# Optimization experiments

Measured on AMD Instinct MI355X. Metric: run time of the kernel, lower is better.

The kernel has to match this reference:

```python
import jax, jax.numpy as jnp
import numpy as np
from jax import lax

EPS = 1e-5
BETA = 0.2  # commitment loss weight


def _conv(x, w, b, stride=2, pad=1):
    # torch Conv2d(k=4, s=2, p=1), NCHW / OIHW
    y = lax.conv_general_dilated(x, w, (stride, stride), [(pad, pad), (pad, pad)],
                                 dimension_numbers=('NCHW', 'OIHW', 'NCHW'))
    return y + b[None, :, None, None]


def _convT(x, w, b):
    # torch ConvTranspose2d(k=4, s=2, p=1): dilated conv with flipped kernel,
    # effective pad = k - 1 - p = 2. w is torch layout [in, out, kH, kW].
    wt = jnp.flip(w, (2, 3)).transpose(1, 0, 2, 3)  # -> [out, in, kH, kW]
    y = lax.conv_general_dilated(x, wt, (1, 1), [(2, 2), (2, 2)], lhs_dilation=(2, 2),
                                 dimension_numbers=('NCHW', 'OIHW', 'NCHW'))
    return y + b[None, :, None, None]


def _bn(x, g, b):
    # BatchNorm2d in training mode: per-channel batch statistics (biased var)
    m = x.mean((0, 2, 3), keepdims=True)
    v = x.var((0, 2, 3), keepdims=True)
    xn = (x - m) * lax.rsqrt(v + EPS)
    return g[None, :, None, None] * xn + b[None, :, None, None]


def _forward(x, enc_w1, enc_b1, enc_w2, enc_b2, enc_w3, enc_b3,
             enc_g1, enc_be1, enc_g2, enc_be2, enc_g3, enc_be3,
             codebook,
             dec_w1, dec_b1, dec_w2, dec_b2, dec_w3, dec_b3,
             dec_g1, dec_be1, dec_g2, dec_be2, dec_g3, dec_be3):
    # ---- Encoder: [B,1,256,256] -> [B,32,32,32] ----
    h = jax.nn.relu(_bn(_conv(x, enc_w1, enc_b1), enc_g1, enc_be1))
    h = jax.nn.relu(_bn(_conv(h, enc_w2, enc_b2), enc_g2, enc_be2))
    q_in = jax.nn.relu(_bn(_conv(h, enc_w3, enc_b3), enc_g3, enc_be3))

    B, C, H, W = q_in.shape
    # ---- Quantiser: cdist + argmin + codebook gather ----
    z = q_in.transpose(0, 2, 3, 1).reshape(B, H * W, C)  # [B, HW, C]
    # squared euclidean distance (same argmin as torch.cdist)
    d2 = (jnp.sum(z * z, -1, keepdims=True)
          - 2.0 * jnp.einsum('bnc,kc->bnk', z, codebook)
          + jnp.sum(codebook * codebook, -1))  # [B, HW, K]
    idx = jnp.argmin(d2, axis=-1)  # [B, HW] int
    q_out = codebook[idx].reshape(B, H, W, C).transpose(0, 3, 1, 2)  # [B,C,H,W]

    commitment = jnp.mean((lax.stop_gradient(q_out) - q_in) ** 2)
    codebook_l = jnp.mean((q_out - lax.stop_gradient(q_in)) ** 2)
    quant_loss = codebook_l + BETA * commitment
    # straight-through estimator
    q_st = q_in + lax.stop_gradient(q_out - q_in)
    encoding_indices = idx.reshape(-1, H, W)

    # ---- Decoder: [B,32,32,32] -> [B,1,256,256] ----
    d = jax.nn.relu(_bn(_convT(q_st, dec_w1, dec_b1), dec_g1, dec_be1))
    d = jax.nn.relu(_bn(_convT(d, dec_w2, dec_b2), dec_g2, dec_be2))
    out = _bn(_convT(d, dec_w3, dec_b3), dec_g3, dec_be3)

    recon = jnp.mean((x - out) ** 2)
    total_loss = quant_loss + recon
    return out, total_loss, encoding_indices


def setup_inputs() -> dict:
    key = jax.random.key(0)
    ks = jax.random.split(key, 12)
    rn = lambda k, s, sc=0.05: jax.random.normal(k, s, jnp.float32) * sc
    inp = {
        'x': jax.random.normal(ks[0], (64, 1, 256, 256), jnp.float32),
        'enc_w1': rn(ks[1], (16, 1, 4, 4)),  'enc_b1': jnp.zeros((16,), jnp.float32),
        'enc_w2': rn(ks[2], (16, 16, 4, 4)), 'enc_b2': jnp.zeros((16,), jnp.float32),
        'enc_w3': rn(ks[3], (32, 16, 4, 4)), 'enc_b3': jnp.zeros((32,), jnp.float32),
        'enc_g1': jnp.ones((16,), jnp.float32), 'enc_be1': jnp.zeros((16,), jnp.float32),
        'enc_g2': jnp.ones((16,), jnp.float32), 'enc_be2': jnp.zeros((16,), jnp.float32),
        'enc_g3': jnp.ones((32,), jnp.float32), 'enc_be3': jnp.zeros((32,), jnp.float32),
        'codebook': jax.random.normal(ks[4], (512, 32), jnp.float32),  # nn.Embedding ~ N(0,1)
        'dec_w1': rn(ks[5], (32, 16, 4, 4)), 'dec_b1': jnp.zeros((16,), jnp.float32),  # [in,out,kH,kW]
        'dec_w2': rn(ks[6], (16, 16, 4, 4)), 'dec_b2': jnp.zeros((16,), jnp.float32),
        'dec_w3': rn(ks[7], (16, 1, 4, 4)),  'dec_b3': jnp.zeros((1,), jnp.float32),
        'dec_g1': jnp.ones((16,), jnp.float32), 'dec_be1': jnp.zeros((16,), jnp.float32),
        'dec_g2': jnp.ones((16,), jnp.float32), 'dec_be2': jnp.zeros((16,), jnp.float32),
        'dec_g3': jnp.ones((1,), jnp.float32),  'dec_be3': jnp.zeros((1,), jnp.float32),
    }
    return inp


def reference(x, enc_w1, enc_b1, enc_w2, enc_b2, enc_w3, enc_b3,
              enc_g1, enc_be1, enc_g2, enc_be2, enc_g3, enc_be3,
              codebook,
              dec_w1, dec_b1, dec_w2, dec_b2, dec_w3, dec_b3,
              dec_g1, dec_be1, dec_g2, dec_be2, dec_g3, dec_be3):
    return _forward(x, enc_w1, enc_b1, enc_w2, enc_b2, enc_w3, enc_b3,
                    enc_g1, enc_be1, enc_g2, enc_be2, enc_g3, enc_be3,
                    codebook,
                    dec_w1, dec_b1, dec_w2, dec_b2, dec_w3, dec_b3,
                    dec_g1, dec_be1, dec_g2, dec_be2, dec_g3, dec_be3)
```

## Files before the change

kernel.cpp:

```cpp
#include <hip/hip_runtime.h>

#define BLK 256


__device__ __forceinline__ void block_stats2(float s, float q, float* partOut) {
  __shared__ float red2[2][4];
  const int lane = threadIdx.x & 63;
  const int wv   = threadIdx.x >> 6;
#pragma unroll
  for (int off = 32; off > 0; off >>= 1) {
    s += __shfl_down(s, off, 64);
    q += __shfl_down(q, off, 64);
  }
  if (lane == 0) { red2[0][wv] = s; red2[1][wv] = q; }
  __syncthreads();
  if (threadIdx.x == 0) {
    partOut[0] = red2[0][0] + red2[0][1] + red2[0][2] + red2[0][3];
    partOut[1] = red2[1][0] + red2[1][1] + red2[1][2] + red2[1][3];
  }
}


__global__ __launch_bounds__(BLK) void twc_k(const float* __restrict__ w,
                                             float* __restrict__ wt,
                                             int CI, int CO) {
  const int total = CI * CO * 16;
  for (int i = threadIdx.x; i < total; i += BLK) {
    const int co = i % CO;
    const int rest = i / CO;
    const int kw = rest & 3, kh = (rest >> 2) & 3, ci = rest >> 4;
    wt[i] = w[(co * CI + ci) * 16 + kh * 4 + kw];
  }
}

__global__ __launch_bounds__(BLK) void twt_k(const float* __restrict__ w,
                                             float* __restrict__ wt,
                                             int CI, int CO) {
  const int total = CI * CO * 16;
  for (int i = threadIdx.x; i < total; i += BLK) {
    const int co = i % CO;
    const int rest = i / CO;
    const int kw = rest & 3, kh = (rest >> 2) & 3, ci = rest >> 4;
    wt[i] = w[(ci * CO + co) * 16 + kh * 4 + kw];
  }
}


template<int CI, int CO, int CGN, int PW, int HIN, int WIN, bool BN_IN>
__global__ __launch_bounds__(64 * PW * CGN) void conv_cg(
    const float* __restrict__ in, const float* __restrict__ wt,
    const float* __restrict__ bias,
    const float* __restrict__ scIn, const float* __restrict__ shIn,
    float* __restrict__ out, float* __restrict__ part)
{
  constexpr int HOUT = HIN / 2, WOUT = WIN / 2;
  constexpr int COG = CO / CGN;
  const int lane = threadIdx.x & 63;
  const int w    = threadIdx.x >> 6;
  const int pw   = w & (PW - 1);
  const int cg   = w / PW;
  const int co0  = __builtin_amdgcn_readfirstlane(cg * COG);

  float sc[CI], sh[CI];
  if constexpr (BN_IN) {
#pragma unroll
    for (int ci = 0; ci < CI; ++ci) { sc[ci] = scIn[ci]; sh[ci] = shIn[ci]; }
  }

  const int pos = blockIdx.x * (64 * PW) + pw * 64 + lane;
  const int ow  = pos % WOUT;
  const int oh  = (pos / WOUT) % HOUT;
  const int b   = pos / (WOUT * HOUT);

  float acc[COG];
#pragma unroll
  for (int j = 0; j < COG; ++j) acc[j] = bias[co0 + j];

  const float* inb = in + (size_t)b * CI * HIN * WIN;

#pragma unroll
  for (int kh = 0; kh < 4; ++kh) {
    const int ih = oh * 2 - 1 + kh;
    if ((unsigned)ih < (unsigned)HIN) {
#pragma unroll
      for (int kw = 0; kw < 4; ++kw) {
        const int iw = ow * 2 - 1 + kw;
        if ((unsigned)iw < (unsigned)WIN) {
#pragma unroll 2
          for (int ci = 0; ci < CI; ++ci) {
            float v = inb[(ci * HIN + ih) * WIN + iw];
            if constexpr (BN_IN) v = fmaxf(fmaf(sc[ci], v, sh[ci]), 0.f);
            const float* wrow = wt + ((ci * 4 + kh) * 4 + kw) * CO + co0;
#pragma unroll
            for (int j = 0; j < COG; ++j)
              acc[j] = fmaf(v, wrow[j], acc[j]);
          }
        }
      }
    }
  }

#pragma unroll
  for (int j = 0; j < COG; ++j)
    out[((size_t)(b * CO + co0 + j) * HOUT + oh) * WOUT + ow] = acc[j];

  float s[COG], q[COG];
#pragma unroll
  for (int j = 0; j < COG; ++j) { s[j] = acc[j]; q[j] = acc[j] * acc[j]; }
#pragma unroll
  for (int off = 32; off > 0; off >>= 1)
#pragma unroll
    for (int j = 0; j < COG; ++j) {
      s[j] += __shfl_down(s[j], off, 64);
      q[j] += __shfl_down(q[j], off, 64);
    }
  __shared__ float red[CGN * PW][COG][2];
  if (lane == 0) {
#pragma unroll
    for (int j = 0; j < COG; ++j) { red[w][j][0] = s[j]; red[w][j][1] = q[j]; }
  }
  __syncthreads();
  if (threadIdx.x < CO) {
    const int co = threadIdx.x;
    const int cg2 = co / COG, j = co % COG;
    float ss = 0.f, qq = 0.f;
#pragma unroll
    for (int p2 = 0; p2 < PW; ++p2) {
      ss += red[cg2 * PW + p2][j][0];
      qq += red[cg2 * PW + p2][j][1];
    }
    part[(size_t)blockIdx.x * CO * 2 + co * 2]     = ss;
    part[(size_t)blockIdx.x * CO * 2 + co * 2 + 1] = qq;
  }
}


template<int CI, int CGN, int PW, int HIN, bool BN_IN>
__global__ __launch_bounds__(64 * PW * CGN) void convTq_cg(
    const float* __restrict__ in, const float* __restrict__ wt,
    const float* __restrict__ bias,
    const float* __restrict__ scIn, const float* __restrict__ shIn,
    float* __restrict__ out, float* __restrict__ part)
{
  constexpr int WIN = HIN, HOUT = 2 * HIN, WOUT = 2 * WIN;
  constexpr int COG = 16 / CGN;
  const int lane = threadIdx.x & 63;
  const int w    = threadIdx.x >> 6;
  const int pw   = w & (PW - 1);
  const int cg   = w / PW;
  const int co0  = __builtin_amdgcn_readfirstlane(cg * COG);

  const int q_  = blockIdx.x * (64 * PW) + pw * 64 + lane;
  const int qw  = q_ % WIN;
  const int qh  = (q_ / WIN) % HIN;
  const int b   = q_ / (WIN * HIN);

  constexpr int KH[2][2] = {{1, 3}, {0, 2}};
  constexpr int PR[2][2] = {{1, 0}, {2, 1}};

  float acc[2][2][COG];
#pragma unroll
  for (int j = 0; j < COG; ++j) {
    const float bv = bias[co0 + j];
    acc[0][0][j] = bv; acc[0][1][j] = bv;
    acc[1][0][j] = bv; acc[1][1][j] = bv;
  }

  const float* inb = in + (size_t)b * CI * HIN * WIN;

#pragma unroll 2
  for (int ci = 0; ci < CI; ++ci) {
    float sci, shi;
    if constexpr (BN_IN) { sci = scIn[ci]; shi = shIn[ci]; }
    const float* base = inb + ci * HIN * WIN;
    float v[3][3];
#pragma unroll
    for (int pr = 0; pr < 3; ++pr) {
      const int ih = qh - 1 + pr;
      const bool okr = (unsigned)ih < (unsigned)HIN;
#pragma unroll
      for (int pc = 0; pc < 3; ++pc) {
        const int iw = qw - 1 + pc;
        float val = 0.f;
        if (okr && (unsigned)iw < (unsigned)WIN) {
          val = base[ih * WIN + iw];
          if constexpr (BN_IN) val = fmaxf(fmaf(sci, val, shi), 0.f);
        }
        v[pr][pc] = val;
      }
    }
#pragma unroll
    for (int py = 0; py < 2; ++py)
#pragma unroll
      for (int tr = 0; tr < 2; ++tr) {
        const int kh = KH[py][tr], pr_ = PR[py][tr];
#pragma unroll
        for (int px = 0; px < 2; ++px)
#pragma unroll
          for (int tc = 0; tc < 2; ++tc) {
            const int kw = KH[px][tc], pc_ = PR[px][tc];
            const float* wrow = wt + ((ci * 4 + kh) * 4 + kw) * 16 + co0;
            const float pv = v[pr_][pc_];
#pragma unroll
            for (int j = 0; j < COG; ++j)
              acc[py][px][j] = fmaf(pv, wrow[j], acc[py][px][j]);
          }
      }
  }

  float* ob = out + (size_t)b * 16 * HOUT * WOUT;
#pragma unroll
  for (int j = 0; j < COG; ++j)
#pragma unroll
    for (int py = 0; py < 2; ++py) {
      float2 o; o.x = acc[py][0][j]; o.y = acc[py][1][j];
      *(float2*)&ob[((size_t)(co0 + j) * HOUT + 2 * qh + py) * WOUT + 2 * qw] = o;
    }

  float s[COG], q[COG];
#pragma unroll
  for (int j = 0; j < COG; ++j) {
    float a = acc[0][0][j] + acc[0][1][j] + acc[1][0][j] + acc[1][1][j];
    float qq = acc[0][0][j] * acc[0][0][j];
    qq = fmaf(acc[0][1][j], acc[0][1][j], qq);
    qq = fmaf(acc[1][0][j], acc[1][0][j], qq);
    qq = fmaf(acc[1][1][j], acc[1][1][j], qq);
    s[j] = a; q[j] = qq;
  }
#pragma unroll
  for (int off = 32; off > 0; off >>= 1)
#pragma unroll
    for (int j = 0; j < COG; ++j) {
      s[j] += __shfl_down(s[j], off, 64);
      q[j] += __shfl_down(q[j], off, 64);
    }
  __shared__ float red[CGN * PW][COG][2];
  if (lane == 0) {
#pragma unroll
    for (int j = 0; j < COG; ++j) { red[w][j][0] = s[j]; red[w][j][1] = q[j]; }
  }
  __syncthreads();
  if (threadIdx.x < 16) {
    const int co = threadIdx.x;
    const int cg2 = co / COG, j = co % COG;
    float ss = 0.f, qq = 0.f;
#pragma unroll
    for (int p2 = 0; p2 < PW; ++p2) {
      ss += red[cg2 * PW + p2][j][0];
      qq += red[cg2 * PW + p2][j][1];
    }
    part[(size_t)blockIdx.x * 32 + co * 2]     = ss;
    part[(size_t)blockIdx.x * 32 + co * 2 + 1] = qq;
  }
}


__global__ __launch_bounds__(BLK) void convT3q_k(
    const float* __restrict__ in, const float* __restrict__ w,
    const float* __restrict__ bias,
    const float* __restrict__ scIn, const float* __restrict__ shIn,
    float* __restrict__ out, float* __restrict__ part)
{
  __shared__ float wl[256];
  wl[threadIdx.x] = w[threadIdx.x];
  float sc[16], sh[16];
#pragma unroll
  for (int ci = 0; ci < 16; ++ci) { sc[ci] = scIn[ci]; sh[ci] = shIn[ci]; }
  const float b0 = bias[0];
  __syncthreads();

  const int idx = blockIdx.x * BLK + threadIdx.x;
  const int tx = idx & 63;
  const int ty = (idx >> 6) & 63;
  const int b  = idx >> 12;
  const int i0 = ty * 2, j0 = tx * 2;

  constexpr int TAP[4][4] = {{1,1,3,0},{0,2,2,1},{1,2,3,1},{0,3,2,2}};

  float acc[4][4];
#pragma unroll
  for (int r = 0; r < 4; ++r)
#pragma unroll
    for (int c = 0; c < 4; ++c) acc[r][c] = b0;

  const float* inb = in + (size_t)b * 16 * 16384;

#pragma unroll 4
  for (int ci = 0; ci < 16; ++ci) {
    const float sci = sc[ci], shi = sh[ci];
    const float* base = inb + ci * 16384;
    float v[4][4];
#pragma unroll
    for (int pr = 0; pr < 4; ++pr) {
      const int ih = i0 - 1 + pr;
      const bool okr = (unsigned)ih < 128u;
#pragma unroll
      for (int pc = 0; pc < 4; ++pc) {
        const int iw = j0 - 1 + pc;
        float val = 0.f;
        if (okr && (unsigned)iw < 128u)
          val = fmaxf(fmaf(sci, base[ih * 128 + iw], shi), 0.f);
        v[pr][pc] = val;
      }
    }
    const float4 w0 = *(const float4*)&wl[ci * 16 + 0];
    const float4 w1 = *(const float4*)&wl[ci * 16 + 4];
    const float4 w2 = *(const float4*)&wl[ci * 16 + 8];
    const float4 w3 = *(const float4*)&wl[ci * 16 + 12];
    const float wg[16] = {w0.x,w0.y,w0.z,w0.w, w1.x,w1.y,w1.z,w1.w,
                          w2.x,w2.y,w2.z,w2.w, w3.x,w3.y,w3.z,w3.w};
#pragma unroll
    for (int r = 0; r < 4; ++r) {
      const int k1r = TAP[r][0], p1r = TAP[r][1], k2r = TAP[r][2], p2r = TAP[r][3];
#pragma unroll
      for (int c = 0; c < 4; ++c) {
        const int k1c = TAP[c][0], p1c = TAP[c][1], k2c = TAP[c][2], p2c = TAP[c][3];
        float a = acc[r][c];
        a = fmaf(v[p1r][p1c], wg[k1r * 4 + k1c], a);
        a = fmaf(v[p1r][p2c], wg[k1r * 4 + k2c], a);
        a = fmaf(v[p2r][p1c], wg[k2r * 4 + k1c], a);
        a = fmaf(v[p2r][p2c], wg[k2r * 4 + k2c], a);
        acc[r][c] = a;
      }
    }
  }

  float* ob = out + (size_t)b * 65536;
#pragma unroll
  for (int r = 0; r < 4; ++r) {
    float4 o;
    o.x = acc[r][0]; o.y = acc[r][1]; o.z = acc[r][2]; o.w = acc[r][3];
    *(float4*)&ob[(ty * 4 + r) * 256 + tx * 4] = o;
  }

  float s = 0.f, q = 0.f;
#pragma unroll
  for (int r = 0; r < 4; ++r)
#pragma unroll
    for (int c = 0; c < 4; ++c) { s += acc[r][c]; q = fmaf(acc[r][c], acc[r][c], q); }
  block_stats2(s, q, part + (size_t)blockIdx.x * 2);
}


template<int C>
__global__ __launch_bounds__(BLK) void stats_k(
    const float* __restrict__ part, int nB, double N,
    const float* __restrict__ g, const float* __restrict__ be,
    float* __restrict__ sc, float* __restrict__ sh)
{
  const int c = blockIdx.x;
  double s0 = 0.0, s1 = 0.0;
  for (int i = threadIdx.x; i < nB; i += BLK) {
    s0 += (double)part[(size_t)i * C * 2 + c * 2];
    s1 += (double)part[(size_t)i * C * 2 + c * 2 + 1];
  }
  __shared__ double lds[8];
  const int lane = threadIdx.x & 63, wv = threadIdx.x >> 6;
#pragma unroll
  for (int off = 32; off > 0; off >>= 1) {
    s0 += __shfl_down(s0, off, 64);
    s1 += __shfl_down(s1, off, 64);
  }
  if (lane == 0) { lds[wv * 2] = s0; lds[wv * 2 + 1] = s1; }
  __syncthreads();
  if (threadIdx.x == 0) {
    s0 = lds[0] + lds[2] + lds[4] + lds[6];
    s1 = lds[1] + lds[3] + lds[5] + lds[7];
    const double mean = s0 / N;
    const double var  = s1 / N - mean * mean;
    const double inv  = 1.0 / sqrt(var + 1e-5);
    sc[c] = (float)((double)g[c] * inv);
    sh[c] = (float)((double)be[c] - mean * (double)g[c] * inv);
  }
}


__global__ __launch_bounds__(BLK) void cbn_k(const float* __restrict__ cbg,
                                             float* __restrict__ cbn)
{
  const int k = blockIdx.x * BLK + threadIdx.x;
  float s = 0.f;
#pragma unroll
  for (int c = 0; c < 32; ++c) {
    const float x = cbg[k * 32 + c];
    s = fmaf(x, x, s);
  }
  cbn[k] = s;
}

__global__ __launch_bounds__(BLK) void quantp_k(
    const float* __restrict__ y3, const float* __restrict__ cbg,
    const float* __restrict__ cbnG,
    const float* __restrict__ sc, const float* __restrict__ sh,
    float* __restrict__ bd, int* __restrict__ bki)
{
  __shared__ float cb[64 * 32];
  __shared__ float cbnl[64];
  const int pblk  = blockIdx.x & 63;
  const int chunk = blockIdx.x >> 6;
  for (int i = threadIdx.x; i < 2048; i += BLK) cb[i] = cbg[chunk * 2048 + i];
  if (threadIdx.x < 64) cbnl[threadIdx.x] = cbnG[chunk * 64 + threadIdx.x];
  __syncthreads();

  const int pos0 = pblk * 1024 + threadIdx.x;

  float z[4][32];
#pragma unroll
  for (int c = 0; c < 32; ++c) {
    const float s_ = sc[c], h_ = sh[c];
#pragma unroll
    for (int j = 0; j < 4; ++j) {
      const int pos = pos0 + j * 256;
      const int bb = pos >> 10, pp = pos & 1023;
      z[j][c] = fmaxf(fmaf(s_, y3[((size_t)(bb * 32 + c)) * 1024 + pp], h_), 0.f);
    }
  }

  float best[4] = {3.402823466e38f, 3.402823466e38f, 3.402823466e38f, 3.402823466e38f};
  int   bk[4]   = {0, 0, 0, 0};

  for (int k = 0; k < 64; ++k) {
    const float4* row = (const float4*)&cb[k * 32];
    float d[4] = {0.f, 0.f, 0.f, 0.f};
#pragma unroll
    for (int c4 = 0; c4 < 8; ++c4) {
      const float4 cc = row[c4];
#pragma unroll
      for (int j = 0; j < 4; ++j) {
        d[j] = fmaf(z[j][c4 * 4 + 0], cc.x, d[j]);
        d[j] = fmaf(z[j][c4 * 4 + 1], cc.y, d[j]);
        d[j] = fmaf(z[j][c4 * 4 + 2], cc.z, d[j]);
        d[j] = fmaf(z[j][c4 * 4 + 3], cc.w, d[j]);
      }
    }
    const float cl = cbnl[k];
    const int kk = chunk * 64 + k;
#pragma unroll
    for (int j = 0; j < 4; ++j) {
      const float dd = cl - 2.f * d[j];
      if (dd < best[j]) { best[j] = dd; bk[j] = kk; }
    }
  }

#pragma unroll
  for (int j = 0; j < 4; ++j) {
    const int pos = pos0 + j * 256;
    bd[chunk * 65536 + pos]  = best[j];
    bki[chunk * 65536 + pos] = bk[j];
  }
}

__global__ __launch_bounds__(BLK) void quantm_k(
    const float* __restrict__ y3, const float* __restrict__ cbg,
    const float* __restrict__ sc, const float* __restrict__ sh,
    const float* __restrict__ bd, const int* __restrict__ bki,
    float* __restrict__ qout, float* __restrict__ idx_out,
    float* __restrict__ pq)
{
  const int pos = blockIdx.x * BLK + threadIdx.x;
  float best = 3.402823466e38f;
  int bk = 0;
#pragma unroll
  for (int s = 0; s < 8; ++s) {
    const float d = bd[s * 65536 + pos];
    const int   k = bki[s * 65536 + pos];
    if (d < best) { best = d; bk = k; }
  }

  const int b = pos >> 10, p = pos & 1023;
  const float4* qrow = (const float4*)(cbg + (size_t)bk * 32);
  float msd = 0.f;
#pragma unroll
  for (int c4 = 0; c4 < 8; ++c4) {
    const float4 q4 = qrow[c4];
    const float qv[4] = {q4.x, q4.y, q4.z, q4.w};
#pragma unroll
    for (int u = 0; u < 4; ++u) {
      const int c = c4 * 4 + u;
      const float v  = y3[((size_t)(b * 32 + c)) * 1024 + p];
      const float zz = fmaxf(fmaf(sc[c], v, sh[c]), 0.f);
      const float qq = qv[u];
      qout[((size_t)(b * 32 + c)) * 1024 + p] = zz + (qq - zz);
      const float df = qq - zz;
      msd = fmaf(df, df, msd);
    }
  }
  idx_out[pos] = (float)bk;
  block_stats2(msd, 0.f, pq + (size_t)blockIdx.x * 2);
}


__global__ __launch_bounds__(BLK) void final4_k(
    const float* __restrict__ y6, const float* __restrict__ x,
    const float* __restrict__ sc, const float* __restrict__ sh,
    float* __restrict__ out, float* __restrict__ pr)
{
  const size_t i = ((size_t)blockIdx.x * BLK + threadIdx.x) * 4;
  const float s0 = sc[0], h0 = sh[0];
  const float4 yv = *(const float4*)(y6 + i);
  const float4 xv = *(const float4*)(x + i);
  float4 ov;
  ov.x = fmaf(s0, yv.x, h0);
  ov.y = fmaf(s0, yv.y, h0);
  ov.z = fmaf(s0, yv.z, h0);
  ov.w = fmaf(s0, yv.w, h0);
  *(float4*)(out + i) = ov;
  const float d0 = xv.x - ov.x, d1 = xv.y - ov.y, d2 = xv.z - ov.z, d3 = xv.w - ov.w;
  float s = d0 * d0;
  s = fmaf(d1, d1, s);
  s = fmaf(d2, d2, s);
  s = fmaf(d3, d3, s);
  block_stats2(s, 0.f, pr + (size_t)blockIdx.x * 2);
}


__global__ __launch_bounds__(BLK) void loss_k(
    const float* __restrict__ pq, const float* __restrict__ pr,
    float* __restrict__ lossOut)
{
  double s = 0.0, r = 0.0;
  for (int i = threadIdx.x; i < 256; i += BLK)  s += (double)pq[i * 2];
  for (int i = threadIdx.x; i < 4096; i += BLK) r += (double)pr[i * 2];
  __shared__ double lds[8];
  const int lane = threadIdx.x & 63, wv = threadIdx.x >> 6;
#pragma unroll
  for (int off = 32; off > 0; off >>= 1) {
    s += __shfl_down(s, off, 64);
    r += __shfl_down(r, off, 64);
  }
  if (lane == 0) { lds[wv * 2] = s; lds[wv * 2 + 1] = r; }
  __syncthreads();
  if (threadIdx.x == 0) {
    s = lds[0] + lds[2] + lds[4] + lds[6];
    r = lds[1] + lds[3] + lds[5] + lds[7];
    lossOut[0] = (float)(1.2 * (s / 2097152.0) + r / 4194304.0);
  }
}


extern "C" void kernel_launch(void* const* d_in, const int* in_sizes, int n_in,
                              void* d_out, int out_size, void* d_ws, size_t ws_size,
                              hipStream_t stream) {
  const float* x    = (const float*)d_in[0];
  const float* ew1  = (const float*)d_in[1];
  const float* eb1  = (const float*)d_in[2];
  const float* ew2  = (const float*)d_in[3];
  const float* eb2  = (const float*)d_in[4];
  const float* ew3  = (const float*)d_in[5];
  const float* eb3  = (const float*)d_in[6];
  const float* eg1  = (const float*)d_in[7];
  const float* ebe1 = (const float*)d_in[8];
  const float* eg2  = (const float*)d_in[9];
  const float* ebe2 = (const float*)d_in[10];
  const float* eg3  = (const float*)d_in[11];
  const float* ebe3 = (const float*)d_in[12];
  const float* cbk  = (const float*)d_in[13];
  const float* dw1  = (const float*)d_in[14];
  const float* db1  = (const float*)d_in[15];
  const float* dw2  = (const float*)d_in[16];
  const float* db2  = (const float*)d_in[17];
  const float* dw3  = (const float*)d_in[18];
  const float* db3  = (const float*)d_in[19];
  const float* dg1  = (const float*)d_in[20];
  const float* dbe1 = (const float*)d_in[21];
  const float* dg2  = (const float*)d_in[22];
  const float* dbe2 = (const float*)d_in[23];
  const float* dg3  = (const float*)d_in[24];
  const float* dbe3 = (const float*)d_in[25];

  float* ws = (float*)d_ws;
  float* outp = (float*)d_out;

  float* SC = ws;
  float* SH = ws + 192;
  float* P1 = ws + 1024;
  float* P2 = ws + 132096;
  float* P3 = ws + 164864;
  float* P4 = ws + 181248;
  float* P5 = ws + 214016;
  float* P6 = ws + 345088;
  float* Pq = ws + 377856;
  float* Pr = ws + 378368;
  float* CBN = ws + 411648;
  float* WT1  = ws + 412160;
  float* WT2  = WT1 + 256;
  float* WT3  = WT2 + 4096;
  float* WTD1 = WT3 + 8192;
  float* WTD2 = WTD1 + 8192;

  float* y1 = ws + 524288;
  float* y2 = y1 + 16777216;
  float* y3 = y2 + 4194304;
  float* qo = y3 + 2097152;
  float* y6 = qo + 2097152;
  float* y4 = y2;
  float* y5 = y1;
  float* bd  = y2;
  int*   bki = (int*)(y2 + 524288);

  float* sc1 = SC + 0,  *sh1 = SH + 0;
  float* sc2 = SC + 32, *sh2 = SH + 32;
  float* sc3 = SC + 64, *sh3 = SH + 64;
  float* sc4 = SC + 96, *sh4 = SH + 96;
  float* sc5 = SC + 128,*sh5 = SH + 128;
  float* sc6 = SC + 160,*sh6 = SH + 160;

  twc_k<<<1, BLK, 0, stream>>>(ew1, WT1, 1, 16);
  twc_k<<<1, BLK, 0, stream>>>(ew2, WT2, 16, 16);
  twc_k<<<1, BLK, 0, stream>>>(ew3, WT3, 16, 32);
  twt_k<<<1, BLK, 0, stream>>>(dw1, WTD1, 32, 16);
  twt_k<<<1, BLK, 0, stream>>>(dw2, WTD2, 16, 16);
  cbn_k<<<2, BLK, 0, stream>>>(cbk, CBN);

  conv_cg<1, 16, 2, 4, 256, 256, false><<<4096, 512, 0, stream>>>(x,  WT1, eb1, nullptr, nullptr, y1, P1);
  stats_k<16><<<16, BLK, 0, stream>>>(P1, 4096, 1048576.0, eg1, ebe1, sc1, sh1);
  conv_cg<16, 16, 2, 4, 128, 128, true><<<1024, 512, 0, stream>>>(y1, WT2, eb2, sc1, sh1, y2, P2);
  stats_k<16><<<16, BLK, 0, stream>>>(P2, 1024, 262144.0, eg2, ebe2, sc2, sh2);
  conv_cg<16, 32, 4, 4, 64, 64, true><<<256, 1024, 0, stream>>>(y2, WT3, eb3, sc2, sh2, y3, P3);
  stats_k<32><<<32, BLK, 0, stream>>>(P3, 256, 65536.0, eg3, ebe3, sc3, sh3);

  quantp_k<<<512, BLK, 0, stream>>>(y3, cbk, CBN, sc3, sh3, bd, bki);
  quantm_k<<<256, BLK, 0, stream>>>(y3, cbk, sc3, sh3, bd, bki, qo, outp + 4194305, Pq);

  convTq_cg<32, 4, 1, 32, false><<<1024, 256, 0, stream>>>(qo, WTD1, db1, nullptr, nullptr, y4, P4);
  stats_k<16><<<16, BLK, 0, stream>>>(P4, 1024, 262144.0, dg1, dbe1, sc4, sh4);
  convTq_cg<16, 2, 2, 64, true><<<2048, 256, 0, stream>>>(y4, WTD2, db2, sc4, sh4, y5, P5);
  stats_k<16><<<16, BLK, 0, stream>>>(P5, 2048, 1048576.0, dg2, dbe2, sc5, sh5);
  convT3q_k<<<1024, BLK, 0, stream>>>(y5, dw3, db3, sc5, sh5, y6, P6);
  stats_k<1><<<1, BLK, 0, stream>>>(P6, 1024, 4194304.0, dg3, dbe3, sc6, sh6);

  final4_k<<<4096, BLK, 0, stream>>>(y6, x, sc6, sh6, outp, Pr);
  loss_k<<<1, BLK, 0, stream>>>(Pq, Pr, outp + 4194304);
}
```

Measured before the change: 621.8 us.

## Compute two output rows per thread in encoder convs and decoder convT

Adds conv_cg2 and convTq2_cg variants where each thread computes two output rows (or a 2x2x2 output block for the transposed conv). Overlapping input rows are loaded once and reused across both, and grid sizes are halved to match. This cuts redundant global input loads and BN-apply work per output, at the cost of more accumulator registers and fewer blocks. convT3q_k also drops its LDS weight staging and the barrier, reading weights directly from global memory, which relies on uniform scalar or cached loads.

```diff
diff --git a/kernel.cpp b/kernel.cpp
--- a/kernel.cpp
+++ b/kernel.cpp
@@ -47,6 +47,119 @@
 
 
 template<int CI, int CO, int CGN, int PW, int HIN, int WIN, bool BN_IN>
+__global__ __launch_bounds__(64 * PW * CGN) void conv_cg2(
+    const float* __restrict__ in, const float* __restrict__ wt,
+    const float* __restrict__ bias,
+    const float* __restrict__ scIn, const float* __restrict__ shIn,
+    float* __restrict__ out, float* __restrict__ part)
+{
+  constexpr int HOUT = HIN / 2, WOUT = WIN / 2;
+  constexpr int COG = CO / CGN;
+  const int lane = threadIdx.x & 63;
+  const int w    = threadIdx.x >> 6;
+  const int pw   = w & (PW - 1);
+  const int cg   = w / PW;
+  const int co0  = __builtin_amdgcn_readfirstlane(cg * COG);
+
+  float sc[CI], sh[CI];
+  if constexpr (BN_IN) {
+#pragma unroll
+    for (int ci = 0; ci < CI; ++ci) { sc[ci] = scIn[ci]; sh[ci] = shIn[ci]; }
+  }
+
+  const int pp  = blockIdx.x * (64 * PW) + pw * 64 + lane;
+  const int ow  = pp % WOUT;
+  const int op  = (pp / WOUT) % (HOUT / 2);
+  const int b   = pp / (WOUT * (HOUT / 2));
+  const int ih0 = 4 * op - 1;
+  const int iw0 = 2 * ow - 1;
+
+  float acc[2][COG];
+#pragma unroll
+  for (int j = 0; j < COG; ++j) {
+    const float bv = bias[co0 + j];
+    acc[0][j] = bv; acc[1][j] = bv;
+  }
+
+  const float* inb = in + (size_t)b * CI * HIN * WIN;
+
+#pragma unroll 2
+  for (int ci = 0; ci < CI; ++ci) {
+    float sci, shi;
+    if constexpr (BN_IN) { sci = sc[ci]; shi = sh[ci]; }
+    const float* base = inb + ci * HIN * WIN;
+    float v[6][4];
+#pragma unroll
+    for (int pr = 0; pr < 6; ++pr) {
+      const int ih = ih0 + pr;
+      const bool okr = (unsigned)ih < (unsigned)HIN;
+#pragma unroll
+      for (int pc = 0; pc < 4; ++pc) {
+        const int iw = iw0 + pc;
+        float val = 0.f;
+        if (okr && (unsigned)iw < (unsigned)WIN) {
+          val = base[ih * WIN + iw];
+          if constexpr (BN_IN) val = fmaxf(fmaf(sci, val, shi), 0.f);
+        }
+        v[pr][pc] = val;
+      }
+    }
+#pragma unroll
+    for (int r2 = 0; r2 < 2; ++r2)
+#pragma unroll
+      for (int kh = 0; kh < 4; ++kh)
+#pragma unroll
+        for (int kw = 0; kw < 4; ++kw) {
+          const float pv = v[2 * r2 + kh][kw];
+          const float* wrow = wt + ((ci * 4 + kh) * 4 + kw) * CO + co0;
+#pragma unroll
+          for (int j = 0; j < COG; ++j)
+            acc[r2][j] = fmaf(pv, wrow[j], acc[r2][j]);
+        }
+  }
+
+#pragma unroll
+  for (int r2 = 0; r2 < 2; ++r2)
+#pragma unroll
+    for (int j = 0; j < COG; ++j)
+      out[((size_t)(b * CO + co0 + j) * HOUT + 2 * op + r2) * WOUT + ow] = acc[r2][j];
+
+  float s[COG], q[COG];
+#pragma unroll
+  for (int j = 0; j < COG; ++j) {
+    s[j] = acc[0][j] + acc[1][j];
+    float qq = acc[0][j] * acc[0][j];
+    q[j] = fmaf(acc[1][j], acc[1][j], qq);
+  }
+#pragma unroll
+  for (int off = 32; off > 0; off >>= 1)
+#pragma unroll
+    for (int j = 0; j < COG; ++j) {
+      s[j] += __shfl_down(s[j], off, 64);
+      q[j] += __shfl_down(q[j], off, 64);
+    }
+  __shared__ float red[CGN * PW][COG][2];
+  if (lane == 0) {
+#pragma unroll
+    for (int j = 0; j < COG; ++j) { red[w][j][0] = s[j]; red[w][j][1] = q[j]; }
+  }
+  __syncthreads();
+  if (threadIdx.x < CO) {
+    const int co = threadIdx.x;
+    const int cg2 = co / COG, j = co % COG;
+    float ss = 0.f, qq = 0.f;
+#pragma unroll
+    for (int p2 = 0; p2 < PW; ++p2) {
+      ss += red[cg2 * PW + p2][j][0];
+      qq += red[cg2 * PW + p2][j][1];
+    }
+    part[(size_t)blockIdx.x * CO * 2 + co * 2]     = ss;
+    part[(size_t)blockIdx.x * CO * 2 + co * 2 + 1] = qq;
+  }
+}
+
+
+template<int CI, int CO, int CGN, int PW, int HIN, int WIN, bool BN_IN>
 __global__ __launch_bounds__(64 * PW * CGN) void conv_cg(
     const float* __restrict__ in, const float* __restrict__ wt,
     const float* __restrict__ bias,
@@ -255,19 +368,150 @@
 }
 
 
+template<int CI, int CGN, int PW, int HIN, bool BN_IN>
+__global__ __launch_bounds__(64 * PW * CGN) void convTq2_cg(
+    const float* __restrict__ in, const float* __restrict__ wt,
+    const float* __restrict__ bias,
+    const float* __restrict__ scIn, const float* __restrict__ shIn,
+    float* __restrict__ out, float* __restrict__ part)
+{
+  constexpr int WIN = HIN, HOUT = 2 * HIN, WOUT = 2 * WIN;
+  constexpr int COG = 16 / CGN;
+  const int lane = threadIdx.x & 63;
+  const int w    = threadIdx.x >> 6;
+  const int pw   = w & (PW - 1);
+  const int cg   = w / PW;
+  const int co0  = __builtin_amdgcn_readfirstlane(cg * COG);
+
+  const int q_  = blockIdx.x * (64 * PW) + pw * 64 + lane;
+  const int qw  = q_ % WIN;
+  const int tq  = (q_ / WIN) % (HIN / 2);
+  const int b   = q_ / (WIN * (HIN / 2));
+  const int qh0 = 2 * tq;
+
+  constexpr int KH[2][2] = {{1, 3}, {0, 2}};
+  constexpr int PR[2][2] = {{1, 0}, {2, 1}};
+
+  float acc[2][2][2][COG];
+#pragma unroll
+  for (int j = 0; j < COG; ++j) {
+    const float bv = bias[co0 + j];
+#pragma unroll
+    for (int t2 = 0; t2 < 2; ++t2)
+#pragma unroll
+      for (int py = 0; py < 2; ++py)
+#pragma unroll
+        for (int px = 0; px < 2; ++px) acc[t2][py][px][j] = bv;
+  }
+
+  const float* inb = in + (size_t)b * CI * HIN * WIN;
+
+#pragma unroll 2
+  for (int ci = 0; ci < CI; ++ci) {
+    float sci, shi;
+    if constexpr (BN_IN) { sci = scIn[ci]; shi = shIn[ci]; }
+    const float* base = inb + ci * HIN * WIN;
+    float v[4][3];
+#pragma unroll
+    for (int pr = 0; pr < 4; ++pr) {
+      const int ih = qh0 - 1 + pr;
+      const bool okr = (unsigned)ih < (unsigned)HIN;
+#pragma unroll
+      for (int pc = 0; pc < 3; ++pc) {
+        const int iw = qw - 1 + pc;
+        float val = 0.f;
+        if (okr && (unsigned)iw < (unsigned)WIN) {
+          val = base[ih * WIN + iw];
+          if constexpr (BN_IN) val = fmaxf(fmaf(sci, val, shi), 0.f);
+        }
+        v[pr][pc] = val;
+      }
+    }
+#pragma unroll
+    for (int t2 = 0; t2 < 2; ++t2)
+#pragma unroll
+      for (int py = 0; py < 2; ++py)
+#pragma unroll
+        for (int tr = 0; tr < 2; ++tr) {
+          const int kh = KH[py][tr], pr_ = t2 + PR[py][tr];
+#pragma unroll
+          for (int px = 0; px < 2; ++px)
+#pragma unroll
+            for (int tc = 0; tc < 2; ++tc) {
+              const int kw = KH[px][tc], pc_ = PR[px][tc];
+              const float* wrow = wt + ((ci * 4 + kh) * 4 + kw) * 16 + co0;
+              const float pv = v[pr_][pc_];
+#pragma unroll
+              for (int j = 0; j < COG; ++j)
+                acc[t2][py][px][j] = fmaf(pv, wrow[j], acc[t2][py][px][j]);
+            }
+        }
+  }
+
+  float* ob = out + (size_t)b * 16 * HOUT * WOUT;
+#pragma unroll
+  for (int j = 0; j < COG; ++j)
+#pragma unroll
+    for (int t2 = 0; t2 < 2; ++t2)
+#pragma unroll
+      for (int py = 0; py < 2; ++py) {
+        float2 o; o.x = acc[t2][py][0][j]; o.y = acc[t2][py][1][j];
+        *(float2*)&ob[((size_t)(co0 + j) * HOUT + 2 * (qh0 + t2) + py) * WOUT + 2 * qw] = o;
+      }
+
+  float s[COG], q[COG];
+#pragma unroll
+  for (int j = 0; j < COG; ++j) {
+    float a = 0.f, qq = 0.f;
+#pragma unroll
+    for (int t2 = 0; t2 < 2; ++t2)
+#pragma unroll
+      for (int py = 0; py < 2; ++py)
+#pragma unroll
+        for (int px = 0; px < 2; ++px) {
+          a += acc[t2][py][px][j];
+          qq = fmaf(acc[t2][py][px][j], acc[t2][py][px][j], qq);
+        }
+    s[j] = a; q[j] = qq;
+  }
+#pragma unroll
+  for (int off = 32; off > 0; off >>= 1)
+#pragma unroll
+    for (int j = 0; j < COG; ++j) {
+      s[j] += __shfl_down(s[j], off, 64);
+      q[j] += __shfl_down(q[j], off, 64);
+    }
+  __shared__ float red[CGN * PW][COG][2];
+  if (lane == 0) {
+#pragma unroll
+    for (int j = 0; j < COG; ++j) { red[w][j][0] = s[j]; red[w][j][1] = q[j]; }
+  }
+  __syncthreads();
+  if (threadIdx.x < 16) {
+    const int co = threadIdx.x;
+    const int cg2 = co / COG, j = co % COG;
+    float ss = 0.f, qq = 0.f;
+#pragma unroll
+    for (int p2 = 0; p2 < PW; ++p2) {
+      ss += red[cg2 * PW + p2][j][0];
+      qq += red[cg2 * PW + p2][j][1];
+    }
+    part[(size_t)blockIdx.x * 32 + co * 2]     = ss;
+    part[(size_t)blockIdx.x * 32 + co * 2 + 1] = qq;
+  }
+}
+
+
 __global__ __launch_bounds__(BLK) void convT3q_k(
     const float* __restrict__ in, const float* __restrict__ w,
     const float* __restrict__ bias,
     const float* __restrict__ scIn, const float* __restrict__ shIn,
     float* __restrict__ out, float* __restrict__ part)
 {
-  __shared__ float wl[256];
-  wl[threadIdx.x] = w[threadIdx.x];
   float sc[16], sh[16];
 #pragma unroll
   for (int ci = 0; ci < 16; ++ci) { sc[ci] = scIn[ci]; sh[ci] = shIn[ci]; }
   const float b0 = bias[0];
-  __syncthreads();
 
   const int idx = blockIdx.x * BLK + threadIdx.x;
   const int tx = idx & 63;
@@ -303,12 +547,7 @@
         v[pr][pc] = val;
       }
     }
-    const float4 w0 = *(const float4*)&wl[ci * 16 + 0];
-    const float4 w1 = *(const float4*)&wl[ci * 16 + 4];
-    const float4 w2 = *(const float4*)&wl[ci * 16 + 8];
-    const float4 w3 = *(const float4*)&wl[ci * 16 + 12];
-    const float wg[16] = {w0.x,w0.y,w0.z,w0.w, w1.x,w1.y,w1.z,w1.w,
-                          w2.x,w2.y,w2.z,w2.w, w3.x,w3.y,w3.z,w3.w};
+    const float* wg = w + ci * 16;
 #pragma unroll
     for (int r = 0; r < 4; ++r) {
       const int k1r = TAP[r][0], p1r = TAP[r][1], k2r = TAP[r][2], p2r = TAP[r][3];
@@ -612,10 +851,10 @@
   twt_k<<<1, BLK, 0, stream>>>(dw2, WTD2, 16, 16);
   cbn_k<<<2, BLK, 0, stream>>>(cbk, CBN);
 
-  conv_cg<1, 16, 2, 4, 256, 256, false><<<4096, 512, 0, stream>>>(x,  WT1, eb1, nullptr, nullptr, y1, P1);
-  stats_k<16><<<16, BLK, 0, stream>>>(P1, 4096, 1048576.0, eg1, ebe1, sc1, sh1);
-  conv_cg<16, 16, 2, 4, 128, 128, true><<<1024, 512, 0, stream>>>(y1, WT2, eb2, sc1, sh1, y2, P2);
-  stats_k<16><<<16, BLK, 0, stream>>>(P2, 1024, 262144.0, eg2, ebe2, sc2, sh2);
+  conv_cg2<1, 16, 2, 4, 256, 256, false><<<2048, 512, 0, stream>>>(x,  WT1, eb1, nullptr, nullptr, y1, P1);
+  stats_k<16><<<16, BLK, 0, stream>>>(P1, 2048, 1048576.0, eg1, ebe1, sc1, sh1);
+  conv_cg2<16, 16, 2, 4, 128, 128, true><<<512, 512, 0, stream>>>(y1, WT2, eb2, sc1, sh1, y2, P2);
+  stats_k<16><<<16, BLK, 0, stream>>>(P2, 512, 262144.0, eg2, ebe2, sc2, sh2);
   conv_cg<16, 32, 4, 4, 64, 64, true><<<256, 1024, 0, stream>>>(y2, WT3, eb3, sc2, sh2, y3, P3);
   stats_k<32><<<32, BLK, 0, stream>>>(P3, 256, 65536.0, eg3, ebe3, sc3, sh3);
 
@@ -624,8 +863,8 @@
 
   convTq_cg<32, 4, 1, 32, false><<<1024, 256, 0, stream>>>(qo, WTD1, db1, nullptr, nullptr, y4, P4);
   stats_k<16><<<16, BLK, 0, stream>>>(P4, 1024, 262144.0, dg1, dbe1, sc4, sh4);
-  convTq_cg<16, 2, 2, 64, true><<<2048, 256, 0, stream>>>(y4, WTD2, db2, sc4, sh4, y5, P5);
-  stats_k<16><<<16, BLK, 0, stream>>>(P5, 2048, 1048576.0, dg2, dbe2, sc5, sh5);
+  convTq2_cg<16, 2, 2, 64, true><<<1024, 256, 0, stream>>>(y4, WTD2, db2, sc4, sh4, y5, P5);
+  stats_k<16><<<16, BLK, 0, stream>>>(P5, 1024, 1048576.0, dg2, dbe2, sc5, sh5);
   convT3q_k<<<1024, BLK, 0, stream>>>(y5, dw3, db3, sc5, sh5, y6, P6);
   stats_k<1><<<1, BLK, 0, stream>>>(P6, 1024, 4194304.0, dg3, dbe3, sc6, sh6);
 
```

Measured after the change: 759.8 us. 1.22x slower.
